# Kernel optimization log

Hardware: AMD Instinct MI355X
Metric: run time of the kernel (lower is better)

Reference implementation:

```python
import jax, jax.numpy as jnp
import numpy as np
from jax import lax

B, N, S, K = 8, 8192, 1024, 32
R2 = 0.2 ** 2
EPS = 1e-5


def _gather(p, idx):
    # p: [B, N, C]; idx: [B, ...] int -> p[b, idx[b]]
    bidx = jnp.arange(p.shape[0]).reshape((p.shape[0],) + (1,) * (idx.ndim - 1))
    return p[bidx, idx]


def _fps(xyz):
    # farthest point sampling; deterministic start at index 0 (torch version uses randint)
    def step(carry, _):
        dist, far = carry
        c = _gather(xyz, far[:, None])            # [B,1,3]
        d = jnp.sum((xyz - c) ** 2, -1)           # [B,N]
        dist = jnp.minimum(dist, d)
        return (dist, jnp.argmax(dist, -1).astype(jnp.int32)), far
    init = (jnp.full(xyz.shape[:2], 1e10, xyz.dtype), jnp.zeros((xyz.shape[0],), jnp.int32))
    _, idx = lax.scan(step, init, None, length=S)
    return idx.T                                   # [B,S]


def _ball_query(xyz, new_xyz):
    # squared dists [B,S,N]
    sq = (jnp.sum(new_xyz ** 2, -1)[:, :, None] + jnp.sum(xyz ** 2, -1)[:, None, :]
          - 2.0 * jnp.einsum('bsc,bnc->bsn', new_xyz, xyz))
    gi = jnp.where(sq > R2, N, jnp.arange(N, dtype=jnp.int32))
    # K smallest indices within radius == K largest of (N - gi); equivalent to sort()[:, :, :K]
    vals, _ = lax.top_k(N - gi, K)
    gi = N - vals                                  # [B,S,K]
    first = gi[:, :, :1]
    return jnp.where(gi == N, first, gi)


def _forward(xyz, points, params):
    xyz = xyz.transpose(0, 2, 1)                   # [B,N,3]
    points = points.transpose(0, 2, 1)             # [B,N,C]
    fps_idx = _fps(xyz)                            # [B,S]
    new_xyz = _gather(xyz, fps_idx)                # [B,S,3]
    gi = _ball_query(xyz, new_xyz)                 # [B,S,K]
    g_xyz = _gather(xyz, gi) - new_xyz[:, :, None, :]            # [B,S,K,3]
    g_pts = jnp.concatenate([_gather(points, gi), g_xyz], -1)    # [B,S,K,C+3]
    x = g_pts.transpose(0, 3, 2, 1)                # [B,C+3,K,S]
    for w, b, g, be in params:
        x = jnp.einsum('oc,bcks->boks', w, x) + b[None, :, None, None]
        m = jnp.mean(x, axis=(0, 2, 3), keepdims=True)
        v = jnp.mean((x - m) ** 2, axis=(0, 2, 3), keepdims=True)  # biased var (BN train mode)
        x = jax.nn.relu(g[None, :, None, None] * (x - m) / jnp.sqrt(v + EPS) + be[None, :, None, None])
    return new_xyz.transpose(0, 2, 1), jnp.max(x, axis=2)          # [B,3,S], [B,128,S]


def setup_inputs() -> dict:
    key = jax.random.key(0)
    ks = jax.random.split(key, 8)
    chans = [(67, 64), (64, 64), (64, 128)]
    inp = {
        'xyz': jax.random.normal(ks[0], (B, 3, N), jnp.float32),
        'points': jax.random.normal(ks[1], (B, 64, N), jnp.float32),
    }
    for i, (ci, co) in enumerate(chans):
        kw = jax.random.fold_in(ks[2], i)
        inp[f'w{i}'] = jax.random.normal(kw, (co, ci), jnp.float32) * 0.1
        inp[f'b{i}'] = jnp.zeros((co,), jnp.float32)
        inp[f'g{i}'] = jnp.ones((co,), jnp.float32)
        inp[f'be{i}'] = jnp.zeros((co,), jnp.float32)
    return inp


def reference(xyz, points, w0, b0, g0, be0, w1, b1, g1, be1, w2, b2, g2, be2):
    params = [(w0, b0, g0, be0), (w1, b1, g1, be1), (w2, b2, g2, be2)]
    return _forward(xyz, points, params)
```

## Files before the change

### kernel.cpp

```cpp
#include <hip/hip_runtime.h>

typedef unsigned short ushort_t;
typedef unsigned int uint_t;
typedef unsigned long long u64_t;
typedef unsigned short us8 __attribute__((ext_vector_type(8)));

constexpr int B_ = 8, N_ = 8192, S_ = 1024, K_ = 32;
constexpr int M_ = B_ * S_ * K_;
constexpr float R2_ = 0.04f;
constexpr float EPS_ = 1e-5f;

__device__ __forceinline__ float bf2f(ushort_t u) {
    union { uint_t i; float f; } v; v.i = ((uint_t)u) << 16; return v.f;
}
__device__ __forceinline__ ushort_t f2bf(float f) {
    union { float f; uint_t i; } v; v.f = f;
    uint_t i = v.i;
    uint_t r = (i + 0x7FFFu + ((i >> 16) & 1u)) >> 16;
    return (ushort_t)r;
}

template<int C> __device__ __forceinline__ float dmaxf(float v) {
    int o = __builtin_amdgcn_mov_dpp(__float_as_int(v), C, 0xf, 0xf, true);
    return fmaxf(v, __int_as_float(o));
}

__global__ __launch_bounds__(1024, 4)
void fps_kernel(const float* __restrict__ xyz, int* __restrict__ fps_idx) {
    constexpr int T = 1024, P = N_ / T;
    const int b = blockIdx.x, t = threadIdx.x;
    const int lane = t & 63, w = t >> 6;
    const float* X = xyz + (size_t)b * 3 * N_;

    __shared__ float4 sxyz[N_];
    __shared__ float rv[16];
    __shared__ int sfar;

#pragma unroll
    for (int i = 0; i < P; ++i) {
        int n = t + i * T;
        sxyz[n] = make_float4(X[n], X[N_ + n], X[2 * N_ + n], 0.0f);
    }
    if (t == 0) fps_idx[b * S_] = 0;
    __syncthreads();

    float px[P], py[P], pz[P], dist[P];
#pragma unroll
    for (int i = 0; i < P; ++i) {
        int j = (i + t) & (P - 1);
        float4 v = sxyz[t * P + j];
        px[j] = v.x; py[j] = v.y; pz[j] = v.z;
        dist[j] = 1e10f;
    }
    float4 cc = sxyz[0];
    float cx = cc.x, cy = cc.y, cz = cc.z;

    for (int s = 0; s < S_; ++s) {
#pragma unroll
        for (int i = 0; i < P; ++i) {
            float dx = __fsub_rn(px[i], cx);
            float dy = __fsub_rn(py[i], cy);
            float dz = __fsub_rn(pz[i], cz);
            float d = __fadd_rn(__fadd_rn(__fmul_rn(dx, dx), __fmul_rn(dy, dy)), __fmul_rn(dz, dz));
            dist[i] = fminf(dist[i], d);
        }
        float a0 = fmaxf(dist[0], dist[4]);
        float a1 = fmaxf(dist[1], dist[5]);
        float a2 = fmaxf(dist[2], dist[6]);
        float a3 = fmaxf(dist[3], dist[7]);
        float lmax = fmaxf(fmaxf(a0, a1), fmaxf(a2, a3));
        float m = lmax;
        m = dmaxf<0x111>(m);
        m = dmaxf<0x112>(m);
        m = dmaxf<0x114>(m);
        m = dmaxf<0x118>(m);
        m = dmaxf<0x142>(m);
        m = dmaxf<0x143>(m);
        if (lane == 63) rv[w] = m;
        __syncthreads();

        float kv0 = rv[lane & 15];
        float kv = kv0;
        kv = dmaxf<0x121>(kv);
        kv = dmaxf<0x122>(kv);
        kv = dmaxf<0x124>(kv);
        kv = dmaxf<0x128>(kv);
        float gmax = kv;
        u64_t wm = __ballot(kv0 == gmax);
        int first_w = __builtin_ctzll(wm);

        if (w == first_w) {
            u64_t lm = __ballot(lmax == gmax);
            int L = __builtin_ctzll(lm);
            if (lane == L) {
                int fi = 0;
#pragma unroll
                for (int i = P - 1; i >= 0; --i)
                    if (dist[i] == gmax) fi = i;
                int nf = t * P + fi;
                sfar = nf;
                if (s + 1 < S_) fps_idx[b * S_ + s + 1] = nf;
            }
        }
        __syncthreads();
        int nf = sfar;
        float4 c = sxyz[nf];
        cx = c.x; cy = c.y; cz = c.z;
    }
}

__global__ __launch_bounds__(256)
void gather_nxyz(const float* __restrict__ xyz, const int* __restrict__ fps_idx,
                 float* __restrict__ nxyz, float* __restrict__ out0) {
    int i = blockIdx.x * 256 + threadIdx.x;
    if (i >= B_ * S_) return;
    int b = i / S_, s = i % S_;
    int idx = fps_idx[i];
    const float* X = xyz + (size_t)b * 3 * N_;
    float x = X[idx], y = X[N_ + idx], z = X[2 * N_ + idx];
    nxyz[(size_t)i * 3 + 0] = x;
    nxyz[(size_t)i * 3 + 1] = y;
    nxyz[(size_t)i * 3 + 2] = z;
    out0[((size_t)b * 3 + 0) * S_ + s] = x;
    out0[((size_t)b * 3 + 1) * S_ + s] = y;
    out0[((size_t)b * 3 + 2) * S_ + s] = z;
}

__global__ __launch_bounds__(256)
void ballq_kernel(const float* __restrict__ xyz, const float* __restrict__ nxyz,
                  int* __restrict__ gi) {
    int wid = (blockIdx.x * 256 + threadIdx.x) >> 6;
    int lane = threadIdx.x & 63;
    if (wid >= B_ * S_) return;
    int b = wid / S_;
    const float* X = xyz + (size_t)b * 3 * N_;
    float nx = nxyz[(size_t)wid * 3 + 0];
    float ny = nxyz[(size_t)wid * 3 + 1];
    float nz = nxyz[(size_t)wid * 3 + 2];
    float snew = __fadd_rn(__fadd_rn(__fmul_rn(nx, nx), __fmul_rn(ny, ny)), __fmul_rn(nz, nz));
    int cnt = 0; int firstn = 0;
    int* out = gi + (size_t)wid * K_;
    for (int c0 = 0; c0 < N_; c0 += 64) {
        int n = c0 + lane;
        float xx = X[n], xy = X[N_ + n], xz = X[2 * N_ + n];
        float sxn = __fadd_rn(__fadd_rn(__fmul_rn(xx, xx), __fmul_rn(xy, xy)), __fmul_rn(xz, xz));
        float dot = __fadd_rn(__fadd_rn(__fmul_rn(nx, xx), __fmul_rn(ny, xy)), __fmul_rn(nz, xz));
        float sq = __fsub_rn(__fadd_rn(snew, sxn), __fmul_rn(2.0f, dot));
        bool inr = !(sq > R2_);
        unsigned long long mask = __ballot(inr);
        if (cnt == 0 && mask) firstn = c0 + __builtin_ctzll(mask);
        int rank = __popcll(mask & ((1ull << lane) - 1ull));
        if (inr && cnt + rank < K_) out[cnt + rank] = n;
        cnt += (int)__popcll(mask);
        if (cnt >= K_) break;
    }
    if (cnt < K_ && lane >= cnt && lane < K_) out[lane] = firstn;
}

__global__ __launch_bounds__(256)
void transpose_pts(const float* __restrict__ pts, ushort_t* __restrict__ ptT) {
    __shared__ ushort_t tile[64][66];
    int b = blockIdx.y; int n0 = blockIdx.x * 64;
    int tc = threadIdx.x & 63;
    int tr = threadIdx.x >> 6;
    const float* src = pts + (size_t)b * 64 * N_;
#pragma unroll
    for (int i = 0; i < 16; ++i) {
        int c = i * 4 + tr;
        tile[c][tc] = f2bf(src[(size_t)c * N_ + n0 + tc]);
    }
    __syncthreads();
#pragma unroll
    for (int i = 0; i < 16; ++i) {
        int nr = i * 4 + tr;
        ptT[((size_t)b * N_ + n0 + nr) * 64 + tc] = tile[tc][nr];
    }
}

__global__ void wt_kernel(const float* __restrict__ w0, const float* __restrict__ w1,
                          const float* __restrict__ w2, float* __restrict__ wt) {
    int l = blockIdx.x;
    const float* w = l == 0 ? w0 : (l == 1 ? w1 : w2);
    int CI = (l == 0) ? 67 : 64;
    int CO = (l == 2) ? 128 : 64;
    float* dst = wt + (l == 0 ? 0 : (l == 1 ? 67 * 64 : 67 * 64 + 64 * 64));
    for (int i = threadIdx.x; i < CI * CO; i += 256) {
        int c = i / CO, o = i % CO;
        dst[c * CO + o] = w[o * CI + c];
    }
}

__global__ __launch_bounds__(256)
void layer1_kernel(const ushort_t* __restrict__ ptT,
                   const float* __restrict__ xyz,
                   const float* __restrict__ nxyz,
                   const int* __restrict__ gi,
                   const float* __restrict__ WT,
                   const float* __restrict__ bias,
                   ushort_t* __restrict__ y) {
    int m = blockIdx.x * 256 + threadIdx.x;
    float acc[64];
#pragma unroll
    for (int o = 0; o < 64; ++o) acc[o] = bias[o];

    int idx = gi[m];
    int b = m >> 15;
    const ushort_t* row = ptT + ((size_t)b * N_ + idx) * 64;
#pragma unroll
    for (int c8 = 0; c8 < 8; ++c8) {
        us8 v = *reinterpret_cast<const us8*>(row + c8 * 8);
#pragma unroll
        for (int j = 0; j < 8; ++j) {
            int c = c8 * 8 + j;
            float h = bf2f(v[j]);
            const float* wr = WT + (size_t)c * 64;
#pragma unroll
            for (int o = 0; o < 64; ++o) acc[o] = fmaf(h, wr[o], acc[o]);
        }
    }
    int s = (m >> 5) & (S_ - 1);
    const float* X = xyz + (size_t)b * 3 * N_;
    const float* nx = nxyz + ((size_t)(b * S_ + s)) * 3;
#pragma unroll
    for (int j = 0; j < 3; ++j) {
        float h = X[(size_t)j * N_ + idx] - nx[j];
        const float* wr = WT + (size_t)(64 + j) * 64;
#pragma unroll
        for (int o = 0; o < 64; ++o) acc[o] = fmaf(h, wr[o], acc[o]);
    }
    ushort_t* yr = y + (size_t)m * 64;
#pragma unroll
    for (int v8 = 0; v8 < 8; ++v8) {
        us8 wv;
#pragma unroll
        for (int j = 0; j < 8; ++j) wv[j] = f2bf(acc[v8 * 8 + j]);
        *reinterpret_cast<us8*>(yr + v8 * 8) = wv;
    }
}

__global__ __launch_bounds__(256, 8)
void layer32_kernel(const ushort_t* __restrict__ xin,
                    const float* __restrict__ WT,
                    const float* __restrict__ bias,
                    const float* __restrict__ abuf,
                    ushort_t* __restrict__ y,
                    int COtot) {
    int m = blockIdx.x * 256 + threadIdx.x;
    int os = blockIdx.y * 32;
    float acc[32];
#pragma unroll
    for (int o = 0; o < 32; ++o) acc[o] = bias[os + o];

    const ushort_t* row = xin + (size_t)m * 64;
#pragma unroll
    for (int c8 = 0; c8 < 8; ++c8) {
        us8 v = *reinterpret_cast<const us8*>(row + c8 * 8);
#pragma unroll
        for (int j = 0; j < 8; ++j) {
            int c = c8 * 8 + j;
            float h = fmaxf(fmaf(abuf[c], bf2f(v[j]), abuf[128 + c]), 0.0f);
            const float* wr = WT + (size_t)c * COtot + os;
#pragma unroll
            for (int o = 0; o < 32; ++o) acc[o] = fmaf(h, wr[o], acc[o]);
        }
    }
    ushort_t* yr = y + (size_t)m * COtot + os;
#pragma unroll
    for (int v8 = 0; v8 < 4; ++v8) {
        us8 wv;
#pragma unroll
        for (int j = 0; j < 8; ++j) wv[j] = f2bf(acc[v8 * 8 + j]);
        *reinterpret_cast<us8*>(yr + v8 * 8) = wv;
    }
}

template<int CO>
__global__ __launch_bounds__(256)
void stats_kernel(const ushort_t* __restrict__ y, float* __restrict__ sums) {
    __shared__ float ls[256];
    int t = threadIdx.x;
    ls[t] = 0.0f;
    __syncthreads();
    int lane = t & 63;
    int wid = blockIdx.x * 4 + (t >> 6);
    int nw = gridDim.x * 4;
    if constexpr (CO == 64) {
        float s = 0, q = 0;
        for (int m = wid; m < M_; m += nw) {
            float v = bf2f(y[(size_t)m * 64 + lane]);
            s += v; q = fmaf(v, v, q);
        }
        atomicAdd(&ls[lane], s); atomicAdd(&ls[128 + lane], q);
    } else {
        float s0 = 0, q0 = 0, s1 = 0, q1 = 0;
        for (int m = wid; m < M_; m += nw) {
            uint_t v = *reinterpret_cast<const uint_t*>(y + (size_t)m * 128 + lane * 2);
            float a = bf2f((ushort_t)(v & 0xffff));
            float c = bf2f((ushort_t)(v >> 16));
            s0 += a; q0 = fmaf(a, a, q0);
            s1 += c; q1 = fmaf(c, c, q1);
        }
        int c0 = lane * 2;
        atomicAdd(&ls[c0], s0); atomicAdd(&ls[c0 + 1], s1);
        atomicAdd(&ls[128 + c0], q0); atomicAdd(&ls[128 + c0 + 1], q1);
    }
    __syncthreads();
    atomicAdd(&sums[t], ls[t]);
}

__global__ void finalize_kernel(const float* __restrict__ sums, const float* __restrict__ g,
                                const float* __restrict__ be, float* __restrict__ ab, int CO) {
    int c = threadIdx.x;
    if (c < CO) {
        float mean = sums[c] * (1.0f / (float)M_);
        float var = sums[128 + c] * (1.0f / (float)M_) - mean * mean;
        float a = g[c] / sqrtf(var + EPS_);
        ab[c] = a;
        ab[128 + c] = be[c] - mean * a;
    }
}

__global__ __launch_bounds__(256)
void final_max(const ushort_t* __restrict__ x3, const float* __restrict__ ab,
               float* __restrict__ out1) {
    int t = threadIdx.x;
    int gw = blockIdx.x * 4 + (t >> 6);
    if (gw >= B_ * S_) return;
    int lane = t & 63;
    int b = gw / S_, s = gw % S_;
    int c0 = lane * 2;
    float a0 = ab[c0], k0 = ab[128 + c0];
    float a1 = ab[c0 + 1], k1 = ab[128 + c0 + 1];
    const ushort_t* base = x3 + (size_t)gw * K_ * 128;
    float m0 = -1e30f, m1 = -1e30f;
#pragma unroll 8
    for (int k = 0; k < K_; ++k) {
        uint_t v = *reinterpret_cast<const uint_t*>(base + k * 128 + c0);
        float f0 = fmaf(bf2f((ushort_t)(v & 0xffff)), a0, k0);
        float f1 = fmaf(bf2f((ushort_t)(v >> 16)), a1, k1);
        m0 = fmaxf(m0, f0); m1 = fmaxf(m1, f1);
    }
    out1[((size_t)b * 128 + c0) * S_ + s] = fmaxf(m0, 0.0f);
    out1[((size_t)b * 128 + c0 + 1) * S_ + s] = fmaxf(m1, 0.0f);
}

extern "C" void kernel_launch(void* const* d_in, const int* in_sizes, int n_in,
                              void* d_out, int out_size, void* d_ws, size_t ws_size,
                              hipStream_t stream) {
    const float* xyz = (const float*)d_in[0];
    const float* pts = (const float*)d_in[1];
    const float* w0 = (const float*)d_in[2];
    const float* b0 = (const float*)d_in[3];
    const float* g0 = (const float*)d_in[4];
    const float* be0 = (const float*)d_in[5];
    const float* w1 = (const float*)d_in[6];
    const float* b1 = (const float*)d_in[7];
    const float* g1 = (const float*)d_in[8];
    const float* be1 = (const float*)d_in[9];
    const float* w2 = (const float*)d_in[10];
    const float* b2 = (const float*)d_in[11];
    const float* g2 = (const float*)d_in[12];
    const float* be2 = (const float*)d_in[13];

    float* out0 = (float*)d_out;
    float* out1 = out0 + (size_t)B_ * 3 * S_;

    char* ws = (char*)d_ws;
    int*      fps   = (int*)(ws + 0);
    float*    nxyz  = (float*)(ws + 32768);
    int*      gi    = (int*)(ws + 131072);
    float*    stats = (float*)(ws + 1179648);
    float*    ab    = (float*)(ws + 1182720);
    float*    wt    = (float*)(ws + 1185792);
    ushort_t* ptT   = (ushort_t*)(ws + 2097152);
    ushort_t* xA    = (ushort_t*)(ws + 10485760);
    ushort_t* xB    = (ushort_t*)(ws + 77594624);

    hipMemsetAsync(stats, 0, 3 * 256 * sizeof(float), stream);
    wt_kernel<<<3, 256, 0, stream>>>(w0, w1, w2, wt);
    transpose_pts<<<dim3(N_ / 64, B_), 256, 0, stream>>>(pts, ptT);
    fps_kernel<<<B_, 1024, 0, stream>>>(xyz, fps);
    gather_nxyz<<<(B_ * S_ + 255) / 256, 256, 0, stream>>>(xyz, fps, nxyz, out0);
    ballq_kernel<<<(B_ * S_) / 4, 256, 0, stream>>>(xyz, nxyz, gi);

    layer1_kernel<<<M_ / 256, 256, 0, stream>>>(ptT, xyz, nxyz, gi, wt, b0, xA);
    stats_kernel<64><<<256, 256, 0, stream>>>(xA, stats + 0);
    finalize_kernel<<<1, 128, 0, stream>>>(stats + 0, g0, be0, ab + 0, 64);

    layer32_kernel<<<dim3(M_ / 256, 2), 256, 0, stream>>>(
        xA, wt + 67 * 64, b1, ab + 0, xB, 64);
    stats_kernel<64><<<256, 256, 0, stream>>>(xB, stats + 256);
    finalize_kernel<<<1, 128, 0, stream>>>(stats + 256, g1, be1, ab + 256, 64);

    layer32_kernel<<<dim3(M_ / 256, 4), 256, 0, stream>>>(
        xB, wt + 67 * 64 + 64 * 64, b2, ab + 256, xA, 128);
    stats_kernel<128><<<256, 256, 0, stream>>>(xA, stats + 512);
    finalize_kernel<<<1, 128, 0, stream>>>(stats + 512, g2, be2, ab + 512, 128);

    final_max<<<(B_ * S_) / 4, 256, 0, stream>>>(xA, ab + 512, out1);
}
```

Baseline: 1.391 ms.

## Fuse BN statistics into layer kernels and gather into FPS kernel

Computes per-channel sum and sum-of-squares for batch norm inside the layer kernels, using a shared-memory copy of each block's bf16 outputs, reduced then atomically added to global sums. This removes three separate stats passes that re-read the large activation buffers. The FPS kernel now keeps the sampled indices in shared memory and writes new_xyz and out0 itself, which drops the gather kernel. The stats memset moves into wt_kernel. The cost is extra LDS use per block, which may lower occupancy, plus more global atomics.

```diff
diff --git a/kernel.cpp b/kernel.cpp
--- a/kernel.cpp
+++ b/kernel.cpp
@@ -26,7 +26,8 @@
 }
 
 __global__ __launch_bounds__(1024, 4)
-void fps_kernel(const float* __restrict__ xyz, int* __restrict__ fps_idx) {
+void fps_kernel(const float* __restrict__ xyz, float* __restrict__ nxyz,
+                float* __restrict__ out0) {
     constexpr int T = 1024, P = N_ / T;
     const int b = blockIdx.x, t = threadIdx.x;
     const int lane = t & 63, w = t >> 6;
@@ -35,13 +36,14 @@
     __shared__ float4 sxyz[N_];
     __shared__ float rv[16];
     __shared__ int sfar;
+    __shared__ int sidx[S_];
 
 #pragma unroll
     for (int i = 0; i < P; ++i) {
         int n = t + i * T;
         sxyz[n] = make_float4(X[n], X[N_ + n], X[2 * N_ + n], 0.0f);
     }
-    if (t == 0) fps_idx[b * S_] = 0;
+    if (t == 0) sidx[0] = 0;
     __syncthreads();
 
     float px[P], py[P], pz[P], dist[P];
@@ -99,7 +101,7 @@
                     if (dist[i] == gmax) fi = i;
                 int nf = t * P + fi;
                 sfar = nf;
-                if (s + 1 < S_) fps_idx[b * S_ + s + 1] = nf;
+                if (s + 1 < S_) sidx[s + 1] = nf;
             }
         }
         __syncthreads();
@@ -107,23 +109,18 @@
         float4 c = sxyz[nf];
         cx = c.x; cy = c.y; cz = c.z;
     }
-}
-
-__global__ __launch_bounds__(256)
-void gather_nxyz(const float* __restrict__ xyz, const int* __restrict__ fps_idx,
-                 float* __restrict__ nxyz, float* __restrict__ out0) {
-    int i = blockIdx.x * 256 + threadIdx.x;
-    if (i >= B_ * S_) return;
-    int b = i / S_, s = i % S_;
-    int idx = fps_idx[i];
-    const float* X = xyz + (size_t)b * 3 * N_;
-    float x = X[idx], y = X[N_ + idx], z = X[2 * N_ + idx];
-    nxyz[(size_t)i * 3 + 0] = x;
-    nxyz[(size_t)i * 3 + 1] = y;
-    nxyz[(size_t)i * 3 + 2] = z;
-    out0[((size_t)b * 3 + 0) * S_ + s] = x;
-    out0[((size_t)b * 3 + 1) * S_ + s] = y;
-    out0[((size_t)b * 3 + 2) * S_ + s] = z;
+
+    __syncthreads();
+    {
+        int s = t;
+        int idx = sidx[s];
+        float4 c = sxyz[idx];
+        size_t base = ((size_t)b * S_ + s) * 3;
+        nxyz[base + 0] = c.x; nxyz[base + 1] = c.y; nxyz[base + 2] = c.z;
+        out0[((size_t)b * 3 + 0) * S_ + s] = c.x;
+        out0[((size_t)b * 3 + 1) * S_ + s] = c.y;
+        out0[((size_t)b * 3 + 2) * S_ + s] = c.z;
+    }
 }
 
 __global__ __launch_bounds__(256)
@@ -178,8 +175,12 @@
 }
 
 __global__ void wt_kernel(const float* __restrict__ w0, const float* __restrict__ w1,
-                          const float* __restrict__ w2, float* __restrict__ wt) {
+                          const float* __restrict__ w2, float* __restrict__ wt,
+                          float* __restrict__ stats) {
     int l = blockIdx.x;
+    if (l == 0) {
+        for (int i = threadIdx.x; i < 768; i += 256) stats[i] = 0.0f;
+    }
     const float* w = l == 0 ? w0 : (l == 1 ? w1 : w2);
     int CI = (l == 0) ? 67 : 64;
     int CO = (l == 2) ? 128 : 64;
@@ -197,8 +198,13 @@
                    const int* __restrict__ gi,
                    const float* __restrict__ WT,
                    const float* __restrict__ bias,
-                   ushort_t* __restrict__ y) {
-    int m = blockIdx.x * 256 + threadIdx.x;
+                   ushort_t* __restrict__ y,
+                   float* __restrict__ sums) {
+    constexpr int RP = 72;
+    __shared__ ushort_t sb[256 * RP];
+    __shared__ float ps[128], pq[128];
+    int tid = threadIdx.x;
+    int m = blockIdx.x * 256 + tid;
     float acc[64];
 #pragma unroll
     for (int o = 0; o < 64; ++o) acc[o] = bias[o];
@@ -235,6 +241,23 @@
 #pragma unroll
         for (int j = 0; j < 8; ++j) wv[j] = f2bf(acc[v8 * 8 + j]);
         *reinterpret_cast<us8*>(yr + v8 * 8) = wv;
+        *reinterpret_cast<us8*>(sb + tid * RP + v8 * 8) = wv;
+    }
+    __syncthreads();
+    if (tid < 128) {
+        int c = tid & 63, half = tid >> 6;
+        float sv = 0.0f, qv = 0.0f;
+        int r0 = half * 128;
+        for (int r = 0; r < 128; ++r) {
+            float v = bf2f(sb[(r0 + r) * RP + c]);
+            sv += v; qv = fmaf(v, v, qv);
+        }
+        ps[tid] = sv; pq[tid] = qv;
+    }
+    __syncthreads();
+    if (tid < 64) {
+        atomicAdd(&sums[tid], ps[tid] + ps[tid + 64]);
+        atomicAdd(&sums[128 + tid], pq[tid] + pq[tid + 64]);
     }
 }
 
@@ -244,8 +267,13 @@
                     const float* __restrict__ bias,
                     const float* __restrict__ abuf,
                     ushort_t* __restrict__ y,
-                    int COtot) {
-    int m = blockIdx.x * 256 + threadIdx.x;
+                    int COtot,
+                    float* __restrict__ sums) {
+    constexpr int RP = 40;
+    __shared__ ushort_t sb[256 * RP];
+    __shared__ float ps[64], pq[64];
+    int tid = threadIdx.x;
+    int m = blockIdx.x * 256 + tid;
     int os = blockIdx.y * 32;
     float acc[32];
 #pragma unroll
@@ -271,41 +299,25 @@
 #pragma unroll
         for (int j = 0; j < 8; ++j) wv[j] = f2bf(acc[v8 * 8 + j]);
         *reinterpret_cast<us8*>(yr + v8 * 8) = wv;
-    }
-}
-
-template<int CO>
-__global__ __launch_bounds__(256)
-void stats_kernel(const ushort_t* __restrict__ y, float* __restrict__ sums) {
-    __shared__ float ls[256];
-    int t = threadIdx.x;
-    ls[t] = 0.0f;
-    __syncthreads();
-    int lane = t & 63;
-    int wid = blockIdx.x * 4 + (t >> 6);
-    int nw = gridDim.x * 4;
-    if constexpr (CO == 64) {
-        float s = 0, q = 0;
-        for (int m = wid; m < M_; m += nw) {
-            float v = bf2f(y[(size_t)m * 64 + lane]);
-            s += v; q = fmaf(v, v, q);
-        }
-        atomicAdd(&ls[lane], s); atomicAdd(&ls[128 + lane], q);
-    } else {
-        float s0 = 0, q0 = 0, s1 = 0, q1 = 0;
-        for (int m = wid; m < M_; m += nw) {
-            uint_t v = *reinterpret_cast<const uint_t*>(y + (size_t)m * 128 + lane * 2);
-            float a = bf2f((ushort_t)(v & 0xffff));
-            float c = bf2f((ushort_t)(v >> 16));
-            s0 += a; q0 = fmaf(a, a, q0);
-            s1 += c; q1 = fmaf(c, c, q1);
-        }
-        int c0 = lane * 2;
-        atomicAdd(&ls[c0], s0); atomicAdd(&ls[c0 + 1], s1);
-        atomicAdd(&ls[128 + c0], q0); atomicAdd(&ls[128 + c0 + 1], q1);
-    }
-    __syncthreads();
-    atomicAdd(&sums[t], ls[t]);
+        *reinterpret_cast<us8*>(sb + tid * RP + v8 * 8) = wv;
+    }
+    __syncthreads();
+    if (tid < 64) {
+        int c = tid & 31, half = tid >> 5;
+        float sv = 0.0f, qv = 0.0f;
+        int r0 = half * 128;
+        for (int r = 0; r < 128; ++r) {
+            float v = bf2f(sb[(r0 + r) * RP + c]);
+            sv += v; qv = fmaf(v, v, qv);
+        }
+        ps[tid] = sv; pq[tid] = qv;
+    }
+    __syncthreads();
+    if (tid < 32) {
+        int cg = os + tid;
+        atomicAdd(&sums[cg], ps[tid] + ps[tid + 32]);
+        atomicAdd(&sums[128 + cg], pq[tid] + pq[tid + 32]);
+    }
 }
 
 __global__ void finalize_kernel(const float* __restrict__ sums, const float* __restrict__ g,
@@ -366,7 +378,6 @@
     float* out1 = out0 + (size_t)B_ * 3 * S_;
 
     char* ws = (char*)d_ws;
-    int*      fps   = (int*)(ws + 0);
     float*    nxyz  = (float*)(ws + 32768);
     int*      gi    = (int*)(ws + 131072);
     float*    stats = (float*)(ws + 1179648);
@@ -376,25 +387,20 @@
     ushort_t* xA    = (ushort_t*)(ws + 10485760);
     ushort_t* xB    = (ushort_t*)(ws + 77594624);
 
-    hipMemsetAsync(stats, 0, 3 * 256 * sizeof(float), stream);
-    wt_kernel<<<3, 256, 0, stream>>>(w0, w1, w2, wt);
+    wt_kernel<<<3, 256, 0, stream>>>(w0, w1, w2, wt, stats);
     transpose_pts<<<dim3(N_ / 64, B_), 256, 0, stream>>>(pts, ptT);
-    fps_kernel<<<B_, 1024, 0, stream>>>(xyz, fps);
-    gather_nxyz<<<(B_ * S_ + 255) / 256, 256, 0, stream>>>(xyz, fps, nxyz, out0);
+    fps_kernel<<<B_, 1024, 0, stream>>>(xyz, nxyz, out0);
     ballq_kernel<<<(B_ * S_) / 4, 256, 0, stream>>>(xyz, nxyz, gi);
 
-    layer1_kernel<<<M_ / 256, 256, 0, stream>>>(ptT, xyz, nxyz, gi, wt, b0, xA);
-    stats_kernel<64><<<256, 256, 0, stream>>>(xA, stats + 0);
+    layer1_kernel<<<M_ / 256, 256, 0, stream>>>(ptT, xyz, nxyz, gi, wt, b0, xA, stats + 0);
     finalize_kernel<<<1, 128, 0, stream>>>(stats + 0, g0, be0, ab + 0, 64);
 
     layer32_kernel<<<dim3(M_ / 256, 2), 256, 0, stream>>>(
-        xA, wt + 67 * 64, b1, ab + 0, xB, 64);
-    stats_kernel<64><<<256, 256, 0, stream>>>(xB, stats + 256);
+        xA, wt + 67 * 64, b1, ab + 0, xB, 64, stats + 256);
     finalize_kernel<<<1, 128, 0, stream>>>(stats + 256, g1, be1, ab + 256, 64);
 
     layer32_kernel<<<dim3(M_ / 256, 4), 256, 0, stream>>>(
-        xB, wt + 67 * 64 + 64 * 64, b2, ab + 256, xA, 128);
-    stats_kernel<128><<<256, 256, 0, stream>>>(xA, stats + 512);
+        xB, wt + 67 * 64 + 64 * 64, b2, ab + 256, xA, 128, stats + 512);
     finalize_kernel<<<1, 128, 0, stream>>>(stats + 512, g2, be2, ab + 512, 128);
 
     final_max<<<(B_ * S_) / 4, 256, 0, stream>>>(xA, ab + 512, out1);
```

Result: faster. 1.214 ms (-12.8%).
